# Kernel optimization log

Hardware: AMD Instinct MI355X
Metric: run time of the kernel (lower is better)

Reference implementation:

```python
import jax, jax.numpy as jnp
import numpy as np
from jax import lax

DEC = [256, 128, 64, 32]
INS = [512, 256, 128, 64]


def _conv2d(x, w, b, pad):
    y = lax.conv_general_dilated(x, w, (1, 1), [(pad, pad), (pad, pad)],
                                 dimension_numbers=('NCHW', 'OIHW', 'NCHW'))
    return y + b[None, :, None, None]


def _conv_transpose2d(x, w_t, b):
    # torch ConvTranspose2d(k=3, stride=2, padding=1, output_padding=1): H -> 2H
    # equivalent to lhs-dilated conv with spatially flipped, IO-transposed kernel
    w = jnp.flip(jnp.transpose(w_t, (1, 0, 2, 3)), (2, 3))  # [out, in, 3, 3]
    y = lax.conv_general_dilated(x, w, (1, 1), [(1, 2), (1, 2)],
                                 lhs_dilation=(2, 2),
                                 dimension_numbers=('NCHW', 'OIHW', 'NCHW'))
    return y + b[None, :, None, None]


def setup_inputs() -> dict:
    key = jax.random.key(0)
    ks = iter(jax.random.split(key, 40))
    d = {}
    d['enc_feat'] = jax.random.normal(next(ks), (8, 512, 16, 16), jnp.float32)
    d['semantic_map'] = jax.random.normal(next(ks), (8, 32, 256, 256), jnp.float32)

    def w(k, shape, fan_in):
        return jax.random.normal(k, shape, jnp.float32) / np.float32(np.sqrt(fan_in))

    for i in range(4):
        d['wt%d' % i] = w(next(ks), (INS[i], DEC[i], 3, 3), INS[i] * 9)  # torch convT layout [in,out,kh,kw]
        d['bt%d' % i] = jnp.zeros((DEC[i],), jnp.float32)
        d['wc%d' % i] = w(next(ks), (DEC[i], DEC[i], 3, 3), DEC[i] * 9)
        d['bc%d' % i] = jnp.zeros((DEC[i],), jnp.float32)
    d['w_attn'] = w(next(ks), (16, 32, 1, 1), 32)
    d['b_attn'] = jnp.zeros((16,), jnp.float32)
    d['w_fin'] = w(next(ks), (1, 16, 1, 1), 16)
    d['b_fin'] = jnp.zeros((1,), jnp.float32)
    return d


def _forward(enc_feat, semantic_map, wts, bts, wcs, bcs, w_attn, b_attn, w_fin, b_fin):
    x = enc_feat
    for i in range(4):
        x = jax.nn.elu(_conv_transpose2d(x, wts[i], bts[i]))
        x = jax.nn.elu(_conv2d(x, wcs[i], bcs[i], 1))
        # skip concats are zero-channel in the only executable config -> identity
    # DynamicSemanticAttention (channel attention over C' = in_ch // 2)
    q = _conv2d(x, w_attn, b_attn, 0)                 # [B, 16, H, W]
    kf = _conv2d(semantic_map, w_attn, b_attn, 0)     # [B, 16, H, W]
    B, C, H, W = q.shape
    qf = q.reshape(B, C, H * W)                        # [B, C', N]
    attn = jnp.einsum('bcn,bdn->bcd', qf, kf.reshape(B, C, H * W))  # [B, C', C']
    attn = jax.nn.softmax(attn, axis=-1)
    fused = jnp.einsum('bcd,bdn->bcn', attn, qf).reshape(B, C, H, W) + q
    return jax.nn.sigmoid(_conv2d(fused, w_fin, b_fin, 0))  # [B, 1, H, W]


def reference(enc_feat, semantic_map, wt0, bt0, wc0, bc0, wt1, bt1, wc1, bc1,
              wt2, bt2, wc2, bc2, wt3, bt3, wc3, bc3, w_attn, b_attn, w_fin, b_fin):
    wts = [wt0, wt1, wt2, wt3]
    bts = [bt0, bt1, bt2, bt3]
    wcs = [wc0, wc1, wc2, wc3]
    bcs = [bc0, bc1, bc2, bc3]
    return _forward(enc_feat, semantic_map, wts, bts, wcs, bcs,
                    w_attn, b_attn, w_fin, b_fin)
```

## Files before the change

kernel.cpp:

```cpp
#include <hip/hip_runtime.h>
#include <hip/hip_bf16.h>
#include <math.h>

typedef _Float16 f16;
typedef _Float16 h8 __attribute__((ext_vector_type(8)));
typedef _Float16 h4 __attribute__((ext_vector_type(4)));
typedef float    f4 __attribute__((ext_vector_type(4)));

__device__ __forceinline__ float elu_f(float v) { return v > 0.f ? v : __expf(v) - 1.f; }
__device__ __forceinline__ float sigmoid_f(float v) { return 1.f / (1.f + __expf(-v)); }

struct PrepDesc { const float* src; unsigned dstOff; int OC; int IC; int tr; };
struct P8 { PrepDesc d[8]; };

__global__ void prep_weights_k(P8 p, f16* __restrict__ wp) {
    unsigned idx = blockIdx.x * 256u + threadIdx.x;
    for (int s = 0; s < 8; ++s) {
        const int IC = p.d[s].IC, OC = p.d[s].OC;
        const unsigned cnt = (unsigned)(OC * 9 * IC);
        if (idx < cnt) {
            const int nicc = IC >> 5;
            const int j    = idx & 7;
            const int lane = (idx >> 3) & 63;
            const int mt   = (idx >> 9) & 1;
            unsigned r = idx >> 10;
            const int tap = r % 9;  r /= 9;
            const int icchunk = r % nicc;
            const int ocg     = r / nicc;
            const int oc = ocg * 32 + mt * 16 + (lane & 15);
            const int ic = icchunk * 32 + (lane >> 4) * 8 + j;
            const float v = p.d[s].tr ? p.d[s].src[((size_t)ic * OC + oc) * 9 + tap]
                                      : p.d[s].src[((size_t)oc * IC + ic) * 9 + tap];
            wp[p.d[s].dstOff + idx] = (f16)v;
            return;
        }
        idx -= cnt;
    }
}

__global__ void enc_transpose_k(const float* __restrict__ enc, f16* __restrict__ out) {
    __shared__ float ts[32][257];
    const int b = blockIdx.x >> 4, cg = blockIdx.x & 15;
    const int tid = threadIdx.x;
    #pragma unroll
    for (int i = 0; i < 32; ++i)
        ts[i][tid] = enc[((size_t)(b * 512 + cg * 32 + i)) * 256 + tid];
    __syncthreads();
    #pragma unroll
    for (int k = 0; k < 4; ++k) {
        h8 v;
        #pragma unroll
        for (int q = 0; q < 8; ++q) v[q] = (f16)ts[k * 8 + q][tid];
        *(h8*)(out + ((size_t)(b * 256 + tid)) * 512 + cg * 32 + k * 8) = v;
    }
}

template<int KS, int C>
__launch_bounds__(256)
__global__ void split_finish_k(const f16* __restrict__ part, const float* __restrict__ bias,
                               f16* __restrict__ out, int tot) {
    const int i4 = (blockIdx.x * 256 + threadIdx.x) * 4;
    float s0 = 0.f, s1 = 0.f, s2 = 0.f, s3 = 0.f;
    #pragma unroll
    for (int k = 0; k < KS; ++k) {
        const h4 v = *(const h4*)(part + (size_t)k * tot + i4);
        s0 += (float)v[0]; s1 += (float)v[1]; s2 += (float)v[2]; s3 += (float)v[3];
    }
    const float4 b4 = *(const float4*)(bias + (i4 & (C - 1)));
    h4 hv = {(f16)elu_f(s0 + b4.x), (f16)elu_f(s1 + b4.y),
             (f16)elu_f(s2 + b4.z), (f16)elu_f(s3 + b4.w)};
    *(h4*)(out + i4) = hv;
}

template<int C, int H, int W, int HT, int WT, int NWN, int KS>
__launch_bounds__(256, 2)
__global__ void conv3_mfma(const f16* __restrict__ in, const f16* __restrict__ wp,
                           const float* __restrict__ bias, f16* __restrict__ out,
                           f16* __restrict__ pout) {
    constexpr int NWR = 4 / NWN;
    constexpr int RH  = HT / NWR;
    constexpr int PIXR = WT + 2;
    constexpr int ROWS = HT + 2;
    constexpr int XB = ROWS * PIXR * 80;
    constexpr int NICC = C / 32;
    constexpr int XTILES = W / WT;
    __shared__ __align__(16) char xlds[XB];

    const int tid = threadIdx.x;
    const int wid = tid >> 6, lane = tid & 63;
    const int ln15 = lane & 15, lg = lane >> 4;
    const int ni = wid % NWN, ri = wid / NWN;
    const int bz = blockIdx.z;
    const int bb = bz / (C / 32), ocg = bz % (C / 32);
    const int oc0 = ocg * 32;
    const int bx = blockIdx.x;
    const int xt = bx % XTILES, ks = bx / XTILES;
    const int h0 = blockIdx.y * HT, w0 = xt * WT;
    const int colb = ni * 16 + ln15;

    f4 acc[RH][2] = {};

    for (int icc = ks * (C / KS); icc < (ks + 1) * (C / KS); icc += 32) {
        __syncthreads();
        for (int t = tid; t < ROWS * PIXR * 4; t += 256) {
            const int g = t & 3, pix = t >> 2;
            const int rr = pix / PIXR, ww = pix - rr * PIXR;
            const int gh = h0 - 1 + rr, gw = w0 - 1 + ww;
            h8 v = {};
            if (gh >= 0 && gh < H && gw >= 0 && gw < W)
                v = *(const h8*)(in + (((size_t)bb * H + gh) * W + gw) * C + icc + g * 8);
            *(h8*)(xlds + pix * 80 + g * 16) = v;
        }
        __syncthreads();

        const f16* wbl = wp + ((size_t)(ocg * NICC + (icc >> 5)) * 18) * 512 + lane * 8;
        #pragma unroll
        for (int dw = 0; dw < 3; ++dw) {
            h8 afd[3][2];
            #pragma unroll
            for (int dh = 0; dh < 3; ++dh)
                #pragma unroll
                for (int mt = 0; mt < 2; ++mt)
                    afd[dh][mt] = *(const h8*)(wbl + ((dh * 3 + dw) * 2 + mt) * 512);
            h8 bfv[RH + 2];
            #pragma unroll
            for (int q = 0; q < RH + 2; ++q)
                bfv[q] = *(const h8*)(xlds + ((ri * RH + q) * PIXR + colb + dw) * 80 + lg * 16);
            #pragma unroll
            for (int r = 0; r < RH; ++r) {
                #pragma unroll
                for (int dh = 0; dh < 3; ++dh) {
                    acc[r][0] = __builtin_amdgcn_mfma_f32_16x16x32_f16(afd[dh][0], bfv[r + dh], acc[r][0], 0, 0, 0);
                    acc[r][1] = __builtin_amdgcn_mfma_f32_16x16x32_f16(afd[dh][1], bfv[r + dh], acc[r][1], 0, 0, 0);
                }
            }
        }
    }

    #pragma unroll
    for (int r = 0; r < RH; ++r) {
        const int oh = h0 + ri * RH + r;
        const int ow = w0 + colb;
        #pragma unroll
        for (int mt = 0; mt < 2; ++mt) {
            const int ocl = mt * 16 + lg * 4;
            const f4 v = acc[r][mt];
            if constexpr (KS > 1) {
                const size_t TOT = (size_t)8 * H * W * C;
                h4 hv = {(f16)v.x, (f16)v.y, (f16)v.z, (f16)v.w};
                *(h4*)(pout + (size_t)ks * TOT +
                       (((size_t)bb * H + oh) * W + ow) * C + oc0 + ocl) = hv;
            } else {
                const float4 b4 = *(const float4*)(bias + oc0 + ocl);
                h4 hv = {(f16)elu_f(v.x + b4.x), (f16)elu_f(v.y + b4.y),
                         (f16)elu_f(v.z + b4.z), (f16)elu_f(v.w + b4.w)};
                *(h4*)(out + (((size_t)bb * H + oh) * W + ow) * C + oc0 + ocl) = hv;
            }
        }
    }
}

template<int IC, int OC, int Hi, int Wi, int KS>
__launch_bounds__(256, 2)
__global__ void convt_mfma(const f16* __restrict__ in, const f16* __restrict__ wp,
                           const float* __restrict__ bias, f16* __restrict__ out,
                           f16* __restrict__ pout) {
    constexpr int HT = 4, WT = 16;
    constexpr int PIXR = WT + 1;
    constexpr int ROWS = HT + 1;
    constexpr int XB = ROWS * PIXR * 80;
    constexpr int NICC = IC / 32;
    constexpr int XTILES = Wi / WT;
    __shared__ __align__(16) char xlds[XB];

    const int tid = threadIdx.x;
    const int wid = tid >> 6, lane = tid & 63;
    const int ln15 = lane & 15, lg = lane >> 4;
    const int iloc = wid;
    const int bz = blockIdx.z;
    const int bb = bz / (OC / 32), ocg = bz % (OC / 32);
    const int oc0 = ocg * 32;
    const int bx = blockIdx.x;
    const int xt = bx % XTILES, ks = bx / XTILES;
    const int i0 = blockIdx.y * HT, j0 = xt * WT;

    f4 acc[4][2] = {};

    for (int icc = ks * (IC / KS); icc < (ks + 1) * (IC / KS); icc += 32) {
        __syncthreads();
        for (int t = tid; t < ROWS * PIXR * 4; t += 256) {
            const int g = t & 3, pix = t >> 2;
            const int rr = pix / PIXR, ww = pix - rr * PIXR;
            const int gh = i0 + rr, gw = j0 + ww;
            h8 v = {};
            if (gh < Hi && gw < Wi)
                v = *(const h8*)(in + (((size_t)bb * Hi + gh) * Wi + gw) * IC + icc + g * 8);
            *(h8*)(xlds + pix * 80 + g * 16) = v;
        }
        __syncthreads();

        const f16* wbl = wp + ((size_t)(ocg * NICC + (icc >> 5)) * 18) * 512 + lane * 8;
        h8 af[9][2];
        #pragma unroll
        for (int tap = 0; tap < 9; ++tap)
            #pragma unroll
            for (int mt = 0; mt < 2; ++mt)
                af[tap][mt] = *(const h8*)(wbl + (tap * 2 + mt) * 512);

        h8 bf[2][2];
        #pragma unroll
        for (int a = 0; a < 2; ++a)
            #pragma unroll
            for (int b = 0; b < 2; ++b)
                bf[a][b] = *(const h8*)(xlds + ((iloc + a) * PIXR + ln15 + b) * 80 + lg * 16);

        #pragma unroll
        for (int p = 0; p < 4; ++p) {
            const int di = p >> 1, dj = p & 1;
            #pragma unroll
            for (int a = 0; a < 2; ++a) {
                if (a > di) continue;
                const int kh = 1 + di - 2 * a;
                #pragma unroll
                for (int b = 0; b < 2; ++b) {
                    if (b > dj) continue;
                    const int kw = 1 + dj - 2 * b;
                    const int tap = kh * 3 + kw;
                    acc[p][0] = __builtin_amdgcn_mfma_f32_16x16x32_f16(af[tap][0], bf[a][b], acc[p][0], 0, 0, 0);
                    acc[p][1] = __builtin_amdgcn_mfma_f32_16x16x32_f16(af[tap][1], bf[a][b], acc[p][1], 0, 0, 0);
                }
            }
        }
    }

    #pragma unroll
    for (int p = 0; p < 4; ++p) {
        const int orow = 2 * (i0 + iloc) + (p >> 1);
        const int ocol = 2 * (j0 + ln15) + (p & 1);
        #pragma unroll
        for (int mt = 0; mt < 2; ++mt) {
            const int ocl = mt * 16 + lg * 4;
            const f4 v = acc[p][mt];
            if constexpr (KS > 1) {
                const size_t TOT = (size_t)8 * (2 * Hi) * (2 * Wi) * OC;
                h4 hv = {(f16)v.x, (f16)v.y, (f16)v.z, (f16)v.w};
                *(h4*)(pout + (size_t)ks * TOT +
                       (((size_t)bb * (2 * Hi) + orow) * (2 * Wi) + ocol) * OC + oc0 + ocl) = hv;
            } else {
                const float4 b4 = *(const float4*)(bias + oc0 + ocl);
                h4 hv = {(f16)elu_f(v.x + b4.x), (f16)elu_f(v.y + b4.y),
                         (f16)elu_f(v.z + b4.z), (f16)elu_f(v.w + b4.w)};
                *(h4*)(out + (((size_t)bb * (2 * Hi) + orow) * (2 * Wi) + ocol) * OC + oc0 + ocl) = hv;
            }
        }
    }
}

#define KCH 128
__launch_bounds__(256)
__global__ void gram_mfma_k(const f16* __restrict__ x3, const float* __restrict__ sem,
                            float* __restrict__ part, float* __restrict__ sums) {
    __shared__ __align__(16) f16 xs[4][32][66];
    __shared__ float pl[4][1024];
    __shared__ float sl[4][64];
    const int b = blockIdx.y, kc = blockIdx.x;
    const int tid = threadIdx.x, wid = tid >> 6, lane = tid & 63;
    const int row = lane & 15, kg = lane >> 4;
    const size_t N = 65536;
    const int p0 = kc * 512 + wid * 128;

    const float* sb = sem + ((size_t)b * 32 + row) * N + p0 + kg * 8;
    const int spx = lane >> 1, shalf = lane & 1;

    f4 acc00 = {}, acc01 = {}, acc10 = {}, acc11 = {};
    float sx0 = 0.f, sx1 = 0.f, ss0 = 0.f, ss1 = 0.f;

    for (int s = 0; s < 4; ++s) {
        const f16* xp = x3 + ((size_t)b * N + p0 + s * 32 + spx) * 32 + shalf * 16;
        const h8 w0 = *(const h8*)xp;
        const h8 w1 = *(const h8*)(xp + 8);
        const float4 f0 = *(const float4*)(sb + s * 32);
        const float4 f1 = *(const float4*)(sb + s * 32 + 4);
        const float4 g0 = *(const float4*)(sb + 16 * N + s * 32);
        const float4 g1 = *(const float4*)(sb + 16 * N + s * 32 + 4);
        *(h8*)&xs[wid][spx][shalf * 16]     = w0;
        *(h8*)&xs[wid][spx][shalf * 16 + 8] = w1;
        h8 a0, a1;
        #pragma unroll
        for (int j = 0; j < 8; ++j) {
            a0[j] = xs[wid][kg * 8 + j][row];
            a1[j] = xs[wid][kg * 8 + j][row + 16];
        }
        const h8 b0 = {(f16)f0.x, (f16)f0.y, (f16)f0.z, (f16)f0.w,
                       (f16)f1.x, (f16)f1.y, (f16)f1.z, (f16)f1.w};
        const h8 b1 = {(f16)g0.x, (f16)g0.y, (f16)g0.z, (f16)g0.w,
                       (f16)g1.x, (f16)g1.y, (f16)g1.z, (f16)g1.w};
        acc00 = __builtin_amdgcn_mfma_f32_16x16x32_f16(a0, b0, acc00, 0, 0, 0);
        acc01 = __builtin_amdgcn_mfma_f32_16x16x32_f16(a0, b1, acc01, 0, 0, 0);
        acc10 = __builtin_amdgcn_mfma_f32_16x16x32_f16(a1, b0, acc10, 0, 0, 0);
        acc11 = __builtin_amdgcn_mfma_f32_16x16x32_f16(a1, b1, acc11, 0, 0, 0);
        #pragma unroll
        for (int q = 0; q < 8; ++q) { sx0 += (float)a0[q]; sx1 += (float)a1[q]; }
        ss0 += (f0.x + f0.y + f0.z + f0.w) + (f1.x + f1.y + f1.z + f1.w);
        ss1 += (g0.x + g0.y + g0.z + g0.w) + (g1.x + g1.y + g1.z + g1.w);
    }

    sx0 += __shfl_xor(sx0, 16); sx0 += __shfl_xor(sx0, 32);
    sx1 += __shfl_xor(sx1, 16); sx1 += __shfl_xor(sx1, 32);
    ss0 += __shfl_xor(ss0, 16); ss0 += __shfl_xor(ss0, 32);
    ss1 += __shfl_xor(ss1, 16); ss1 += __shfl_xor(ss1, 32);

    #pragma unroll
    for (int reg = 0; reg < 4; ++reg) {
        const int c0 = 4 * kg + reg;
        pl[wid][c0 * 32 + row]               = acc00[reg];
        pl[wid][c0 * 32 + 16 + row]          = acc01[reg];
        pl[wid][(16 + c0) * 32 + row]        = acc10[reg];
        pl[wid][(16 + c0) * 32 + 16 + row]   = acc11[reg];
    }
    if (lane < 16) {
        sl[wid][row]      = sx0;
        sl[wid][16 + row] = sx1;
        sl[wid][32 + row] = ss0;
        sl[wid][48 + row] = ss1;
    }
    __syncthreads();

    float* pb = part + ((size_t)b * KCH + kc) * 1024;
    #pragma unroll
    for (int t = tid; t < 1024; t += 256)
        pb[t] = pl[0][t] + pl[1][t] + pl[2][t] + pl[3][t];
    if (tid < 64)
        sums[((size_t)b * KCH + kc) * 64 + tid] = sl[0][tid] + sl[1][tid] + sl[2][tid] + sl[3][tid];
}

__launch_bounds__(256)
__global__ void gram_reduce_k(const float* __restrict__ part, const float* __restrict__ sums,
                              float* __restrict__ part2, float* __restrict__ sums2) {
    const int b = blockIdx.y, g = blockIdx.x;
    const int tid = threadIdx.x;
    const int i4 = tid * 4;
    f4 a = {};
    #pragma unroll 4
    for (int ch = 0; ch < 16; ++ch) {
        const f4 v = *(const f4*)(part + ((size_t)b * KCH + g * 16 + ch) * 1024 + i4);
        a.x += v.x; a.y += v.y; a.z += v.z; a.w += v.w;
    }
    *(f4*)(part2 + ((size_t)b * 8 + g) * 1024 + i4) = a;
    if (tid < 64) {
        float s = 0.f;
        #pragma unroll 4
        for (int ch = 0; ch < 16; ++ch) s += sums[((size_t)b * KCH + g * 16 + ch) * 64 + tid];
        sums2[((size_t)b * 8 + g) * 64 + tid] = s;
    }
}

__launch_bounds__(256)
__global__ void attn_finish_v3(const float* __restrict__ part, const float* __restrict__ sums,
                               const float* __restrict__ wa, const float* __restrict__ ba,
                               const float* __restrict__ wf, const float* __restrict__ bf,
                               float* __restrict__ u, float* __restrict__ cb) {
    __shared__ float G[32][33];
    __shared__ float T[16][33];
    __shared__ float A[16][17];
    __shared__ float Sx[32], Ss[32], px[16], ps[16], v[16];
    const int b = blockIdx.x, tid = threadIdx.x;

    float a4[4] = {0.f, 0.f, 0.f, 0.f};
    for (int p = 0; p < 8; ++p) {
        const float* pp = part + ((size_t)b * 8 + p) * 1024 + tid;
        a4[0] += pp[0]; a4[1] += pp[256]; a4[2] += pp[512]; a4[3] += pp[768];
    }
    #pragma unroll
    for (int q = 0; q < 4; ++q) {
        const int t = tid + q * 256;
        G[t >> 5][t & 31] = a4[q];
    }
    if (tid < 64) {
        float s = 0.f;
        for (int p = 0; p < 8; ++p) s += sums[((size_t)b * 8 + p) * 64 + tid];
        if (tid < 32) Sx[tid] = s; else Ss[tid - 32] = s;
    }
    __syncthreads();
    for (int t = tid; t < 512; t += 256) {
        const int c = t >> 5, f = t & 31;
        float s = 0.f;
        #pragma unroll
        for (int e = 0; e < 32; ++e) s = fmaf(wa[c * 32 + e], G[e][f], s);
        T[c][f] = s;
    }
    if (tid < 32) {
        const int c = tid & 15;
        const float* S = (tid < 16) ? Sx : Ss;
        float s = 0.f;
        #pragma unroll
        for (int e = 0; e < 32; ++e) s = fmaf(wa[c * 32 + e], S[e], s);
        if (tid < 16) px[c] = s; else ps[c] = s;
    }
    __syncthreads();
    {
        const int c = tid >> 4, d = tid & 15;
        float s = 0.f;
        #pragma unroll
        for (int f2 = 0; f2 < 32; ++f2) s = fmaf(T[c][f2], wa[d * 32 + f2], s);
        s += px[c] * ba[d] + ba[c] * ps[d] + 65536.f * ba[c] * ba[d];
        A[c][d] = s;
    }
    __syncthreads();
    if (tid < 16) {
        float m = A[tid][0];
        #pragma unroll
        for (int d = 1; d < 16; ++d) m = fmaxf(m, A[tid][d]);
        float s = 0.f;
        #pragma unroll
        for (int d = 0; d < 16; ++d) { const float e = __expf(A[tid][d] - m); A[tid][d] = e; s += e; }
        const float inv = 1.f / s;
        #pragma unroll
        for (int d = 0; d < 16; ++d) A[tid][d] *= inv;
    }
    __syncthreads();
    if (tid < 16) {
        float s = wf[tid];
        #pragma unroll
        for (int c = 0; c < 16; ++c) s = fmaf(wf[c], A[c][tid], s);
        v[tid] = s;
    }
    __syncthreads();
    if (tid < 32) {
        float s = 0.f;
        #pragma unroll
        for (int d = 0; d < 16; ++d) s = fmaf(v[d], wa[d * 32 + tid], s);
        u[b * 32 + tid] = s;
    }
    if (tid == 0) {
        float s2 = bf[0];
        #pragma unroll
        for (int d = 0; d < 16; ++d) s2 = fmaf(v[d], ba[d], s2);
        cb[b] = s2;
    }
}

__launch_bounds__(256)
__global__ void final_k(const f16* __restrict__ x3, const float* __restrict__ u,
                        const float* __restrict__ cb, float* __restrict__ out) {
    const int b = blockIdx.y;
    const int nn = blockIdx.x * 256 + threadIdx.x;
    const f16* xb = x3 + ((size_t)b * 65536 + nn) * 32;
    const float* ub = u + b * 32;
    float acc = cb[b];
    #pragma unroll
    for (int g = 0; g < 4; ++g) {
        const h8 v = *(const h8*)(xb + g * 8);
        #pragma unroll
        for (int q = 0; q < 8; ++q) acc = fmaf(ub[g * 8 + q], (float)v[q], acc);
    }
    out[(size_t)b * 65536 + nn] = sigmoid_f(acc);
}

extern "C" void kernel_launch(void* const* d_in, const int* in_sizes, int n_in,
                              void* d_out, int out_size, void* d_ws, size_t ws_size,
                              hipStream_t stream) {
    const float* enc   = (const float*)d_in[0];
    const float* sem   = (const float*)d_in[1];
    const float* wt0   = (const float*)d_in[2];
    const float* bt0   = (const float*)d_in[3];
    const float* wc0   = (const float*)d_in[4];
    const float* bc0   = (const float*)d_in[5];
    const float* wt1   = (const float*)d_in[6];
    const float* bt1   = (const float*)d_in[7];
    const float* wc1   = (const float*)d_in[8];
    const float* bc1   = (const float*)d_in[9];
    const float* wt2   = (const float*)d_in[10];
    const float* bt2   = (const float*)d_in[11];
    const float* wc2   = (const float*)d_in[12];
    const float* bc2   = (const float*)d_in[13];
    const float* wt3   = (const float*)d_in[14];
    const float* bt3   = (const float*)d_in[15];
    const float* wc3   = (const float*)d_in[16];
    const float* bc3   = (const float*)d_in[17];
    const float* wattn = (const float*)d_in[18];
    const float* battn = (const float*)d_in[19];
    const float* wfin  = (const float*)d_in[20];
    const float* bfin  = (const float*)d_in[21];

    char* W = (char*)d_ws;
    f16*   actA   = (f16*)(W + 0);
    f16*   actB   = (f16*)(W + 33554432);
    f16*   x3cl   = (f16*)(W + 67108864);
    f16*   pf     = (f16*)(W + 67108864);
    f16*   wp     = (f16*)(W + 100663296);
    f16*   enc_cl = (f16*)(W + 105906176);
    float* part   = (float*)(W + 108003328);
    float* sums   = (float*)(W + 112197632);
    float* part2  = (float*)(W + 112459776);
    float* sums2  = (float*)(W + 112721920);
    float* u      = (float*)(W + 112738304);
    float* cb     = (float*)(W + 112739328);
    float* out    = (float*)d_out;

    P8 p;
    p.d[0] = {wt0, 0u,       256, 512, 1};
    p.d[1] = {wc0, 1179648u, 256, 256, 0};
    p.d[2] = {wt1, 1769472u, 128, 256, 1};
    p.d[3] = {wc1, 2064384u, 128, 128, 0};
    p.d[4] = {wt2, 2211840u,  64, 128, 1};
    p.d[5] = {wc2, 2285568u,  64,  64, 0};
    p.d[6] = {wt3, 2322432u,  32,  64, 1};
    p.d[7] = {wc3, 2340864u,  32,  32, 0};
    prep_weights_k<<<9180, 256, 0, stream>>>(p, wp);
    enc_transpose_k<<<128, 256, 0, stream>>>(enc, enc_cl);

    convt_mfma<512, 256, 16, 16, 4><<<dim3(4, 4, 64), 256, 0, stream>>>(enc_cl, wp, nullptr, nullptr, pf);
    split_finish_k<4, 256><<<2048, 256, 0, stream>>>(pf, bt0, actA, 2097152);
    conv3_mfma<256, 32, 32, 8, 32, 2, 4><<<dim3(4, 4, 64), 256, 0, stream>>>(actA, wp + 1179648, nullptr, nullptr, pf);
    split_finish_k<4, 256><<<2048, 256, 0, stream>>>(pf, bc0, actB, 2097152);
    convt_mfma<256, 128, 32, 32, 2><<<dim3(4, 8, 32), 256, 0, stream>>>(actB, wp + 1769472, nullptr, nullptr, pf);
    split_finish_k<2, 128><<<4096, 256, 0, stream>>>(pf, bt1, actA, 4194304);
    conv3_mfma<128, 64, 64, 4, 64, 4, 2><<<dim3(2, 16, 32), 256, 0, stream>>>(actA, wp + 2064384, nullptr, nullptr, pf);
    split_finish_k<2, 128><<<4096, 256, 0, stream>>>(pf, bc1, actB, 4194304);
    convt_mfma<128, 64, 64, 64, 1>      <<<dim3(4, 16, 16), 256, 0, stream>>>(actB, wp + 2211840, bt2, actA, nullptr);
    conv3_mfma<64, 128, 128, 4, 64, 4, 1><<<dim3(2, 32, 16), 256, 0, stream>>>(actA, wp + 2285568, bc2, actB, nullptr);
    convt_mfma<64, 32, 128, 128, 1>     <<<dim3(8, 32, 8),  256, 0, stream>>>(actB, wp + 2322432, bt3, actA, nullptr);
    conv3_mfma<32, 256, 256, 4, 64, 4, 1><<<dim3(4, 64, 8), 256, 0, stream>>>(actA, wp + 2340864, bc3, x3cl, nullptr);

    gram_mfma_k<<<dim3(KCH, 8), 256, 0, stream>>>(x3cl, sem, part, sums);
    gram_reduce_k<<<dim3(8, 8), 256, 0, stream>>>(part, sums, part2, sums2);
    attn_finish_v3<<<8, 256, 0, stream>>>(part2, sums2, wattn, battn, wfin, bfin, u, cb);
    final_k<<<dim3(256, 8), 256, 0, stream>>>(x3cl, u, cb, out);
}
```

Before: 238.6 us.

## Fuse split-K reduction, bias and ELU into next conv's input staging

Removes the four split_finish kernels: each consumer conv now sums the split-K partial buffers, adds bias and applies ELU while staging its input tile into LDS. The weight-prep and encoder-transpose kernels are also merged into a single launch. This cuts several kernel launches and one full write and read of each activation. In exchange, the partial sums are recomputed for every halo and overlapping tile read, and each consumer reads KS times more data.

```diff
diff --git a/kernel.cpp b/kernel.cpp
--- a/kernel.cpp
+++ b/kernel.cpp
@@ -13,8 +13,26 @@
 struct PrepDesc { const float* src; unsigned dstOff; int OC; int IC; int tr; };
 struct P8 { PrepDesc d[8]; };
 
-__global__ void prep_weights_k(P8 p, f16* __restrict__ wp) {
-    unsigned idx = blockIdx.x * 256u + threadIdx.x;
+__global__ void prep_all_k(P8 p, f16* __restrict__ wp,
+                           const float* __restrict__ enc, f16* __restrict__ enc_cl) {
+    __shared__ float ts[32][257];
+    if (blockIdx.x < 128) {
+        const int b = blockIdx.x >> 4, cg = blockIdx.x & 15;
+        const int tid = threadIdx.x;
+        #pragma unroll
+        for (int i = 0; i < 32; ++i)
+            ts[i][tid] = enc[((size_t)(b * 512 + cg * 32 + i)) * 256 + tid];
+        __syncthreads();
+        #pragma unroll
+        for (int k = 0; k < 4; ++k) {
+            h8 v;
+            #pragma unroll
+            for (int q = 0; q < 8; ++q) v[q] = (f16)ts[k * 8 + q][tid];
+            *(h8*)(enc_cl + ((size_t)(b * 256 + tid)) * 512 + cg * 32 + k * 8) = v;
+        }
+        return;
+    }
+    unsigned idx = (blockIdx.x - 128) * 256u + threadIdx.x;
     for (int s = 0; s < 8; ++s) {
         const int IC = p.d[s].IC, OC = p.d[s].OC;
         const unsigned cnt = (unsigned)(OC * 9 * IC);
@@ -38,45 +56,39 @@
     }
 }
 
-__global__ void enc_transpose_k(const float* __restrict__ enc, f16* __restrict__ out) {
-    __shared__ float ts[32][257];
-    const int b = blockIdx.x >> 4, cg = blockIdx.x & 15;
-    const int tid = threadIdx.x;
-    #pragma unroll
-    for (int i = 0; i < 32; ++i)
-        ts[i][tid] = enc[((size_t)(b * 512 + cg * 32 + i)) * 256 + tid];
-    __syncthreads();
-    #pragma unroll
-    for (int k = 0; k < 4; ++k) {
+template<int SKS>
+__device__ __forceinline__ h8 stage_elem(const f16* __restrict__ in, size_t off,
+                                         size_t srcTot, const float* __restrict__ sbias,
+                                         int ch0) {
+    if constexpr (SKS == 1) {
+        return *(const h8*)(in + off);
+    } else {
+        float s[8];
+        const h8 t0 = *(const h8*)(in + off);
+        #pragma unroll
+        for (int j = 0; j < 8; ++j) s[j] = (float)t0[j];
+        #pragma unroll
+        for (int k = 1; k < SKS; ++k) {
+            const h8 tk = *(const h8*)(in + (size_t)k * srcTot + off);
+            #pragma unroll
+            for (int j = 0; j < 8; ++j) s[j] += (float)tk[j];
+        }
+        const float4 b0 = *(const float4*)(sbias + ch0);
+        const float4 b1 = *(const float4*)(sbias + ch0 + 4);
         h8 v;
-        #pragma unroll
-        for (int q = 0; q < 8; ++q) v[q] = (f16)ts[k * 8 + q][tid];
-        *(h8*)(out + ((size_t)(b * 256 + tid)) * 512 + cg * 32 + k * 8) = v;
-    }
-}
-
-template<int KS, int C>
-__launch_bounds__(256)
-__global__ void split_finish_k(const f16* __restrict__ part, const float* __restrict__ bias,
-                               f16* __restrict__ out, int tot) {
-    const int i4 = (blockIdx.x * 256 + threadIdx.x) * 4;
-    float s0 = 0.f, s1 = 0.f, s2 = 0.f, s3 = 0.f;
-    #pragma unroll
-    for (int k = 0; k < KS; ++k) {
-        const h4 v = *(const h4*)(part + (size_t)k * tot + i4);
-        s0 += (float)v[0]; s1 += (float)v[1]; s2 += (float)v[2]; s3 += (float)v[3];
-    }
-    const float4 b4 = *(const float4*)(bias + (i4 & (C - 1)));
-    h4 hv = {(f16)elu_f(s0 + b4.x), (f16)elu_f(s1 + b4.y),
-             (f16)elu_f(s2 + b4.z), (f16)elu_f(s3 + b4.w)};
-    *(h4*)(out + i4) = hv;
-}
-
-template<int C, int H, int W, int HT, int WT, int NWN, int KS>
+        v[0] = (f16)elu_f(s[0] + b0.x); v[1] = (f16)elu_f(s[1] + b0.y);
+        v[2] = (f16)elu_f(s[2] + b0.z); v[3] = (f16)elu_f(s[3] + b0.w);
+        v[4] = (f16)elu_f(s[4] + b1.x); v[5] = (f16)elu_f(s[5] + b1.y);
+        v[6] = (f16)elu_f(s[6] + b1.z); v[7] = (f16)elu_f(s[7] + b1.w);
+        return v;
+    }
+}
+
+template<int C, int H, int W, int HT, int WT, int NWN, int KS, int SKS>
 __launch_bounds__(256, 2)
 __global__ void conv3_mfma(const f16* __restrict__ in, const f16* __restrict__ wp,
-                           const float* __restrict__ bias, f16* __restrict__ out,
-                           f16* __restrict__ pout) {
+                           const float* __restrict__ bias, const float* __restrict__ sbias,
+                           size_t srcTot, f16* __restrict__ out, f16* __restrict__ pout) {
     constexpr int NWR = 4 / NWN;
     constexpr int RH  = HT / NWR;
     constexpr int PIXR = WT + 2;
@@ -107,8 +119,10 @@
             const int rr = pix / PIXR, ww = pix - rr * PIXR;
             const int gh = h0 - 1 + rr, gw = w0 - 1 + ww;
             h8 v = {};
-            if (gh >= 0 && gh < H && gw >= 0 && gw < W)
-                v = *(const h8*)(in + (((size_t)bb * H + gh) * W + gw) * C + icc + g * 8);
+            if (gh >= 0 && gh < H && gw >= 0 && gw < W) {
+                const size_t off = (((size_t)bb * H + gh) * W + gw) * C + icc + g * 8;
+                v = stage_elem<SKS>(in, off, srcTot, sbias, icc + g * 8);
+            }
             *(h8*)(xlds + pix * 80 + g * 16) = v;
         }
         __syncthreads();
@@ -160,11 +174,11 @@
     }
 }
 
-template<int IC, int OC, int Hi, int Wi, int KS>
+template<int IC, int OC, int Hi, int Wi, int KS, int SKS>
 __launch_bounds__(256, 2)
 __global__ void convt_mfma(const f16* __restrict__ in, const f16* __restrict__ wp,
-                           const float* __restrict__ bias, f16* __restrict__ out,
-                           f16* __restrict__ pout) {
+                           const float* __restrict__ bias, const float* __restrict__ sbias,
+                           size_t srcTot, f16* __restrict__ out, f16* __restrict__ pout) {
     constexpr int HT = 4, WT = 16;
     constexpr int PIXR = WT + 1;
     constexpr int ROWS = HT + 1;
@@ -193,8 +207,10 @@
             const int rr = pix / PIXR, ww = pix - rr * PIXR;
             const int gh = i0 + rr, gw = j0 + ww;
             h8 v = {};
-            if (gh < Hi && gw < Wi)
-                v = *(const h8*)(in + (((size_t)bb * Hi + gh) * Wi + gw) * IC + icc + g * 8);
+            if (gh < Hi && gw < Wi) {
+                const size_t off = (((size_t)bb * Hi + gh) * Wi + gw) * IC + icc + g * 8;
+                v = stage_elem<SKS>(in, off, srcTot, sbias, icc + g * 8);
+            }
             *(h8*)(xlds + pix * 80 + g * 16) = v;
         }
         __syncthreads();
@@ -487,7 +503,6 @@
     f16*   actA   = (f16*)(W + 0);
     f16*   actB   = (f16*)(W + 33554432);
     f16*   x3cl   = (f16*)(W + 67108864);
-    f16*   pf     = (f16*)(W + 67108864);
     f16*   wp     = (f16*)(W + 100663296);
     f16*   enc_cl = (f16*)(W + 105906176);
     float* part   = (float*)(W + 108003328);
@@ -497,6 +512,8 @@
     float* u      = (float*)(W + 112738304);
     float* cb     = (float*)(W + 112739328);
     float* out    = (float*)d_out;
+    f16* pfA = actA;
+    f16* pfB = actB;
 
     P8 p;
     p.d[0] = {wt0, 0u,       256, 512, 1};
@@ -507,21 +524,24 @@
     p.d[5] = {wc2, 2285568u,  64,  64, 0};
     p.d[6] = {wt3, 2322432u,  32,  64, 1};
     p.d[7] = {wc3, 2340864u,  32,  32, 0};
-    prep_weights_k<<<9180, 256, 0, stream>>>(p, wp);
-    enc_transpose_k<<<128, 256, 0, stream>>>(enc, enc_cl);
-
-    convt_mfma<512, 256, 16, 16, 4><<<dim3(4, 4, 64), 256, 0, stream>>>(enc_cl, wp, nullptr, nullptr, pf);
-    split_finish_k<4, 256><<<2048, 256, 0, stream>>>(pf, bt0, actA, 2097152);
-    conv3_mfma<256, 32, 32, 8, 32, 2, 4><<<dim3(4, 4, 64), 256, 0, stream>>>(actA, wp + 1179648, nullptr, nullptr, pf);
-    split_finish_k<4, 256><<<2048, 256, 0, stream>>>(pf, bc0, actB, 2097152);
-    convt_mfma<256, 128, 32, 32, 2><<<dim3(4, 8, 32), 256, 0, stream>>>(actB, wp + 1769472, nullptr, nullptr, pf);
-    split_finish_k<2, 128><<<4096, 256, 0, stream>>>(pf, bt1, actA, 4194304);
-    conv3_mfma<128, 64, 64, 4, 64, 4, 2><<<dim3(2, 16, 32), 256, 0, stream>>>(actA, wp + 2064384, nullptr, nullptr, pf);
-    split_finish_k<2, 128><<<4096, 256, 0, stream>>>(pf, bc1, actB, 4194304);
-    convt_mfma<128, 64, 64, 64, 1>      <<<dim3(4, 16, 16), 256, 0, stream>>>(actB, wp + 2211840, bt2, actA, nullptr);
-    conv3_mfma<64, 128, 128, 4, 64, 4, 1><<<dim3(2, 32, 16), 256, 0, stream>>>(actA, wp + 2285568, bc2, actB, nullptr);
-    convt_mfma<64, 32, 128, 128, 1>     <<<dim3(8, 32, 8),  256, 0, stream>>>(actB, wp + 2322432, bt3, actA, nullptr);
-    conv3_mfma<32, 256, 256, 4, 64, 4, 1><<<dim3(4, 64, 8), 256, 0, stream>>>(actA, wp + 2340864, bc3, x3cl, nullptr);
+    prep_all_k<<<9308, 256, 0, stream>>>(p, wp, enc, enc_cl);
+
+    convt_mfma<512, 256, 16, 16, 4, 1><<<dim3(4, 4, 64), 256, 0, stream>>>(
+        enc_cl, wp, nullptr, nullptr, 0, nullptr, pfA);
+    conv3_mfma<256, 32, 32, 8, 32, 2, 4, 4><<<dim3(4, 4, 64), 256, 0, stream>>>(
+        pfA, wp + 1179648, nullptr, bt0, 2097152, nullptr, pfB);
+    convt_mfma<256, 128, 32, 32, 2, 4><<<dim3(4, 8, 32), 256, 0, stream>>>(
+        pfB, wp + 1769472, nullptr, bc0, 2097152, nullptr, pfA);
+    conv3_mfma<128, 64, 64, 4, 64, 4, 2, 2><<<dim3(2, 16, 32), 256, 0, stream>>>(
+        pfA, wp + 2064384, nullptr, bt1, 4194304, nullptr, pfB);
+    convt_mfma<128, 64, 64, 64, 1, 2><<<dim3(4, 16, 16), 256, 0, stream>>>(
+        pfB, wp + 2211840, bt2, bc1, 4194304, actA, nullptr);
+    conv3_mfma<64, 128, 128, 4, 64, 4, 1, 1><<<dim3(2, 32, 16), 256, 0, stream>>>(
+        actA, wp + 2285568, bc2, nullptr, 0, actB, nullptr);
+    convt_mfma<64, 32, 128, 128, 1, 1><<<dim3(8, 32, 8), 256, 0, stream>>>(
+        actB, wp + 2322432, bt3, nullptr, 0, actA, nullptr);
+    conv3_mfma<32, 256, 256, 4, 64, 4, 1, 1><<<dim3(4, 64, 8), 256, 0, stream>>>(
+        actA, wp + 2340864, bc3, nullptr, 0, x3cl, nullptr);
 
     gram_mfma_k<<<dim3(KCH, 8), 256, 0, stream>>>(x3cl, sem, part, sums);
     gram_reduce_k<<<dim3(8, 8), 256, 0, stream>>>(part, sums, part2, sums2);
```

Result: faster. 227.7 us (-4.5%).
